# Performance work log

Measured on AMD Instinct MI355X. Metric: run time of the kernel, lower is better.

The kernel has to match this reference:

```python
import jax, jax.numpy as jnp
import numpy as np

B, H, K = 4096, 256, 16
INPUT_DIM, XPRIME_DIM = 8, 64
D = INPUT_DIM * XPRIME_DIM  # 512
LN_EPS = 1e-5


def setup_inputs() -> dict:
    key = jax.random.key(0)
    ks = jax.random.split(key, 12)
    s1 = 1.0  # Linear(1, D): fan_in=1
    sD = 1.0 / np.sqrt(D)
    sH = 1.0 / np.sqrt(H)
    return {
        "h_prev_rnn": jax.random.normal(ks[0], (B, H), jnp.float32),
        "x_l": jax.random.normal(ks[1], (B, INPUT_DIM), jnp.float32),
        "x_ext": jax.random.normal(ks[2], (B, K), jnp.float32),
        # stacked per-expert MetaNet params
        "meta_w1": jax.random.uniform(ks[3], (K, D), jnp.float32, -s1, s1),
        "meta_b1": jax.random.uniform(ks[4], (K, D), jnp.float32, -s1, s1),
        "meta_w2": jax.random.uniform(ks[5], (K, D, D), jnp.float32, -sD, sD),
        "meta_b2": jax.random.uniform(ks[6], (K, D), jnp.float32, -sD, sD),
        # gating net
        "gw1": jax.random.uniform(ks[7], (H, H), jnp.float32, -sH, sH),
        "gb1": jax.random.uniform(ks[8], (H,), jnp.float32, -sH, sH),
        "gw2": jax.random.uniform(ks[9], (H, K), jnp.float32, -sH, sH),
        "gb2": jax.random.uniform(ks[10], (K,), jnp.float32, -sH, sH),
        # LayerNorm([input_dim, xprime_dim]) affine params
        "ln_g": jnp.ones((INPUT_DIM, XPRIME_DIM), jnp.float32),
        "ln_b": jnp.zeros((INPUT_DIM, XPRIME_DIM), jnp.float32),
        "theta0": jnp.zeros((1, INPUT_DIM, XPRIME_DIM), jnp.float32),
    }


def reference(h_prev_rnn, x_l, x_ext, meta_w1, meta_b1, meta_w2, meta_b2,
              gw1, gb1, gw2, gb2, ln_g, ln_b, theta0):
    # MetaNet layer1 (Linear(1, D)): scalar input per expert -> [B, K, D]
    h1 = jnp.tanh(x_ext[:, :, None] * meta_w1[None] + meta_b1[None])
    # MetaNet layer2: per-expert DxD GEMM
    h2 = jnp.tanh(jnp.einsum('bkd,kde->bke', h1, meta_w2) + meta_b2[None])
    W = h2.reshape(h2.shape[0], K, INPUT_DIM, XPRIME_DIM)  # [B,K,i,e]
    # LayerNorm over last two dims jointly, affine
    mu = W.mean(axis=(-2, -1), keepdims=True)
    var = W.var(axis=(-2, -1), keepdims=True)
    W = (W - mu) * jax.lax.rsqrt(var + LN_EPS) * ln_g + ln_b
    # gating: softmax over experts (epoch/top_k = None path)
    logits = jnp.tanh(h_prev_rnn @ gw1 + gb1) @ gw2 + gb2
    gates = jax.nn.softmax(logits, axis=-1)  # [B, K]
    theta = jnp.einsum('bk,bkie->bie', gates, W) + theta0  # [B, i, e]
    x_prime = jnp.einsum('bi,bie->be', x_l, theta)  # [B, e]
    return (x_prime, theta)
```

## Files before the change

kernel.cpp:

```cpp
#include <hip/hip_runtime.h>
#include <stdint.h>

#define NB 4096
#define NH 256
#define NK 16
#define ND 512
#define NC 48
#define NM 48
#define RCHEB 7.0f
#define PI_F 3.14159265358979323846f
#define CCPART (NK * 2 * ND * 32)

typedef _Float16 f16;
using half8   = __attribute__((ext_vector_type(8))) _Float16;
using float4v = __attribute__((ext_vector_type(4))) float;

__device__ __forceinline__ float fast_tanh(float x) {
  float e = __builtin_amdgcn_exp2f(x * 2.88539008177793f);
  return 1.0f - 2.0f * __builtin_amdgcn_rcpf(e + 1.0f);
}

__global__ __launch_bounds__(256) void k_gs(
    const float* __restrict__ h_prev,
    const float* __restrict__ gw1, const float* __restrict__ gb1,
    const float* __restrict__ gw2, const float* __restrict__ gb2,
    const float* __restrict__ w1, const float* __restrict__ b1,
    float* __restrict__ gates, float* __restrict__ Sg, float* __restrict__ ctg) {
  __shared__ float sbuf[4096];
  const int t = threadIdx.x;
  const int blk = blockIdx.x;

  if (blk >= 512) {
    const int sb = blk - 512;
    const int k = sb >> 3;
    const int d0 = (sb & 7) * 64;
    if (sb == 0) {
      for (int i = t; i < NM * NC; i += 256) {
        const int m = i / 48, j = i - m * 48;
        const int r = (j * (2 * m + 1)) % 192;
        const float fac = (j == 0 ? 1.0f : 2.0f) * (1.0f / 48.0f);
        ctg[i] = cosf(PI_F * (float)r * (1.0f / 96.0f)) * fac;
      }
    }
    const int dl = t >> 2, mg = t & 3;
    const int d = d0 + dl;
    const float a = w1[k * ND + d];
    const float b = b1[k * ND + d];
    float o[12];
#pragma unroll
    for (int mi = 0; mi < 12; ++mi) {
      const int m = mg * 12 + mi;
      const float cx = cosf(PI_F * (float)(2 * m + 1) * (1.0f / 96.0f));
      o[mi] = fast_tanh(fmaf(a, RCHEB * cx, b));
    }
    float* dst = Sg + ((size_t)k * ND + d) * NM + mg * 12;
    *(float4*)&dst[0] = *(float4*)&o[0];
    *(float4*)&dst[4] = *(float4*)&o[4];
    *(float4*)&dst[8] = *(float4*)&o[8];
    return;
  }

  const int b0 = blk * 8;
  float* sh_h = sbuf;
  float* sh_t = sbuf + 2048;
  for (int r = 0; r < 8; ++r) sh_h[r * 256 + t] = h_prev[(b0 + r) * NH + t];
  __syncthreads();
  float acc[8];
  const float bias = gb1[t];
#pragma unroll
  for (int r = 0; r < 8; ++r) acc[r] = bias;
  for (int i = 0; i < NH; i += 4) {
    const float w0 = gw1[(i + 0) * NH + t];
    const float w1v = gw1[(i + 1) * NH + t];
    const float w2v = gw1[(i + 2) * NH + t];
    const float w3 = gw1[(i + 3) * NH + t];
#pragma unroll
    for (int r = 0; r < 8; ++r) {
      const float4 hv = *(const float4*)&sh_h[r * 256 + i];
      acc[r] += hv.x * w0 + hv.y * w1v + hv.z * w2v + hv.w * w3;
    }
  }
#pragma unroll
  for (int r = 0; r < 8; ++r) sh_t[t * 8 + r] = fast_tanh(acc[r]);
  __syncthreads();
  if (t < 128) {
    const int r = t >> 4, k = t & 15;
    float lg = gb2[k];
    for (int j = 0; j < NH; ++j) lg += sh_t[j * 8 + r] * gw2[j * NK + k];
    float m = lg;
    for (int off = 1; off < 16; off <<= 1) m = fmaxf(m, __shfl_xor(m, off, 16));
    const float e = __builtin_amdgcn_exp2f((lg - m) * 1.44269504f);
    float s = e;
    for (int off = 1; off < 16; off <<= 1) s += __shfl_xor(s, off, 16);
    gates[(b0 + r) * NK + k] = e * __builtin_amdgcn_rcpf(s);
  }
}

__global__ __launch_bounds__(256) void k_coef(
    const float* __restrict__ w2, const float* __restrict__ Sg,
    const float* __restrict__ ctg, float* __restrict__ Cc) {
  __shared__ float Gl[48][68];
  const int t = threadIdx.x;
  const int blk = blockIdx.x;
  const int k = blk >> 5;
  const int e0 = ((blk >> 2) & 7) * 64;
  const int dq = blk & 3;
  const int el = t & 63;
  const int mqu = __builtin_amdgcn_readfirstlane(t >> 6);

  const float* w2p = w2 + ((size_t)k * ND + dq * 128) * ND + e0 + el;
  const float* Sp = Sg + ((size_t)k * ND + dq * 128) * NM + mqu * 12;

  float g[12];
#pragma unroll
  for (int i = 0; i < 12; ++i) g[i] = 0.f;
#pragma unroll 4
  for (int d = 0; d < 128; ++d) {
    const float wv = w2p[(size_t)d * ND];
    const float4 s0 = *(const float4*)&Sp[d * NM];
    const float4 s1 = *(const float4*)&Sp[d * NM + 4];
    const float4 s2 = *(const float4*)&Sp[d * NM + 8];
    g[0] = fmaf(s0.x, wv, g[0]);
    g[1] = fmaf(s0.y, wv, g[1]);
    g[2] = fmaf(s0.z, wv, g[2]);
    g[3] = fmaf(s0.w, wv, g[3]);
    g[4] = fmaf(s1.x, wv, g[4]);
    g[5] = fmaf(s1.y, wv, g[5]);
    g[6] = fmaf(s1.z, wv, g[6]);
    g[7] = fmaf(s1.w, wv, g[7]);
    g[8] = fmaf(s2.x, wv, g[8]);
    g[9] = fmaf(s2.y, wv, g[9]);
    g[10] = fmaf(s2.z, wv, g[10]);
    g[11] = fmaf(s2.w, wv, g[11]);
  }

#pragma unroll
  for (int mi = 0; mi < 12; ++mi) Gl[mqu * 12 + mi][el] = g[mi];
  __syncthreads();

  float cacc[12];
#pragma unroll
  for (int i = 0; i < 12; ++i) cacc[i] = 0.f;
#pragma unroll 4
  for (int m = 0; m < NM; ++m) {
    const float gv = Gl[m][el];
    const float4 c0 = *(const float4*)&ctg[m * 48 + mqu * 12];
    const float4 c1 = *(const float4*)&ctg[m * 48 + mqu * 12 + 4];
    const float4 c2 = *(const float4*)&ctg[m * 48 + mqu * 12 + 8];
    cacc[0] = fmaf(c0.x, gv, cacc[0]);
    cacc[1] = fmaf(c0.y, gv, cacc[1]);
    cacc[2] = fmaf(c0.z, gv, cacc[2]);
    cacc[3] = fmaf(c0.w, gv, cacc[3]);
    cacc[4] = fmaf(c1.x, gv, cacc[4]);
    cacc[5] = fmaf(c1.y, gv, cacc[5]);
    cacc[6] = fmaf(c1.z, gv, cacc[6]);
    cacc[7] = fmaf(c1.w, gv, cacc[7]);
    cacc[8] = fmaf(c2.x, gv, cacc[8]);
    cacc[9] = fmaf(c2.y, gv, cacc[9]);
    cacc[10] = fmaf(c2.z, gv, cacc[10]);
    cacc[11] = fmaf(c2.w, gv, cacc[11]);
  }
  float* Ccq = Cc + (size_t)dq * CCPART;
#pragma unroll
  for (int jj = 0; jj < 12; ++jj) {
    const int j = mqu * 12 + jj;
    Ccq[((size_t)(k * 2 + (j >> 5)) * ND + e0 + el) * 32 + (j & 31)] = cacc[jj];
  }
}

__global__ __launch_bounds__(256) void k_pack(
    const float* __restrict__ Cc, const float* __restrict__ b2,
    f16* __restrict__ Cbf) {
  const int idx = blockIdx.x * 256 + threadIdx.x;
  const int flat8 = idx * 8;
  const int k2 = flat8 >> 14;
  const int rem = flat8 & 16383;
  const int e = rem >> 5, o8 = rem & 31;
  const int j0 = (k2 & 1) * 32 + o8;
  f16 o[8];
  if (j0 >= 48) {
#pragma unroll
    for (int i = 0; i < 8; ++i) o[i] = (f16)0.f;
  } else {
    float v[8];
#pragma unroll
    for (int i = 0; i < 8; ++i) v[i] = 0.f;
#pragma unroll
    for (int p = 0; p < 4; ++p) {
      const float4 u0 = *(const float4*)&Cc[(size_t)p * CCPART + flat8];
      const float4 u1 = *(const float4*)&Cc[(size_t)p * CCPART + flat8 + 4];
      v[0] += u0.x; v[1] += u0.y; v[2] += u0.z; v[3] += u0.w;
      v[4] += u1.x; v[5] += u1.y; v[6] += u1.z; v[7] += u1.w;
    }
    if (((k2 & 1) == 0) && (o8 == 0)) v[0] += b2[(k2 >> 1) * ND + e];
#pragma unroll
    for (int i = 0; i < 8; ++i) o[i] = (f16)v[i];
  }
  *(uint4*)&Cbf[flat8] = *(uint4*)o;
}

__global__ __launch_bounds__(256) void k_eval(
    const f16* __restrict__ Cbf, const float* __restrict__ gates,
    const float* __restrict__ x_ext, const float* __restrict__ x_l,
    const float* __restrict__ ln_g, const float* __restrict__ ln_b,
    const float* __restrict__ theta0, float* __restrict__ out) {
  __shared__ __align__(16) char sm[43264];
  f16* Tlds = (f16*)sm;
  float (*xp)[8][68] = (float(*)[8][68])sm;
  float (*lnbuf)[8][4][2] = (float(*)[8][4][2])(sm + 36864);
  float (*sx)[16] = (float(*)[16])(sm + 40960);
  float (*sg)[16] = (float(*)[16])(sm + 41472);
  float (*sxl)[8] = (float(*)[8])(sm + 41984);
  const int t = threadIdx.x;
  const int l = t & 63, wn = t >> 6;
  const int q = l >> 4, m16 = l & 15;
  const int b0 = blockIdx.x * 8;

  const f16* Bbase = Cbf + ((size_t)(wn * 128 + m16)) * 32 + q * 8;
  half8 BrA[16], BrB[16];
  auto loadB = [&](int k, half8(&dst)[16]) {
#pragma unroll
    for (int bni = 0; bni < 8; ++bni) {
      dst[bni * 2 + 0] =
          *(const half8*)(Bbase + ((size_t)(k * 2 + 0) * ND + bni * 16) * 32);
      dst[bni * 2 + 1] =
          *(const half8*)(Bbase + ((size_t)(k * 2 + 1) * ND + bni * 16) * 32);
    }
  };
  loadB(0, BrA);

  if (t < 128) {
    const int row = t >> 4, kk = t & 15;
    sx[row][kk] = x_ext[(b0 + row) * NK + kk];
    sg[row][kk] = gates[(b0 + row) * NK + kk];
  } else if (t < 192) {
    const int tt = t - 128;
    sxl[tt >> 3][tt & 7] = x_l[(b0 + (tt >> 3)) * 8 + (tt & 7)];
  }
  __syncthreads();

  if (t < 128) {
    const int kk = t >> 3, row = t & 7;
    f16* T0 = &Tlds[(2 * kk) * 576 + row * 36];
    f16* T1 = &Tlds[(2 * kk + 1) * 576 + row * 36];
    float u = sx[row][kk] * (1.0f / RCHEB);
    u = fminf(1.0f, fmaxf(-1.0f, u));
    const float u2 = u + u;
    float tp = 1.0f, tc = u;
    T0[0] = (f16)1.0f;
    T0[1] = (f16)u;
#pragma unroll
    for (int j = 2; j < 48; ++j) {
      const float tn = fmaf(u2, tc, -tp);
      tp = tc; tc = tn;
      if (j < 32) T0[j] = (f16)tn; else T1[j - 32] = (f16)tn;
    }
#pragma unroll
    for (int j = 48; j < 64; ++j) T1[j - 32] = (f16)0.f;
  } else {
    const int tt = t - 128;
    const int ksub = tt >> 2;
    f16* Z = &Tlds[ksub * 576 + (8 + (tt & 3) * 2) * 36];
#pragma unroll
    for (int j = 0; j < 72; ++j) Z[j] = (f16)0.f;
  }
  __syncthreads();

  float lng[8], lnb[8];
#pragma unroll
  for (int bni = 0; bni < 8; ++bni) {
    const int col = wn * 128 + bni * 16 + m16;
    lng[bni] = ln_g[col];
    lnb[bni] = ln_b[col];
  }

  float th[8][4];
#pragma unroll
  for (int bni = 0; bni < 8; ++bni)
#pragma unroll
    for (int rr = 0; rr < 4; ++rr) th[bni][rr] = 0.f;

  const f16* Abase = Tlds + m16 * 36 + q * 8;
  const float4v z = {0.f, 0.f, 0.f, 0.f};

  auto stepA = [&](int k, const half8(&Br)[16], float4v(&acc)[8],
                   float(&s)[4], float(&s2)[4]) {
    const half8 a0 = *(const half8*)(Abase + (2 * k) * 576);
    const half8 a1 = *(const half8*)(Abase + (2 * k + 1) * 576);
#pragma unroll
    for (int bni = 0; bni < 8; ++bni) {
      acc[bni] = __builtin_amdgcn_mfma_f32_16x16x32_f16(a0, Br[2 * bni], z, 0, 0, 0);
      acc[bni] = __builtin_amdgcn_mfma_f32_16x16x32_f16(a1, Br[2 * bni + 1],
                                                        acc[bni], 0, 0, 0);
    }
#pragma unroll
    for (int rr = 0; rr < 4; ++rr) { s[rr] = 0.f; s2[rr] = 0.f; }
#pragma unroll
    for (int bni = 0; bni < 8; ++bni)
#pragma unroll
      for (int rr = 0; rr < 4; ++rr) {
        const float v = fast_tanh(acc[bni][rr]);
        acc[bni][rr] = v;
        s[rr] += v;
        s2[rr] = fmaf(v, v, s2[rr]);
      }
#pragma unroll
    for (int off = 1; off < 16; off <<= 1)
#pragma unroll
      for (int rr = 0; rr < 4; ++rr) {
        s[rr] += __shfl_xor(s[rr], off, 64);
        s2[rr] += __shfl_xor(s2[rr], off, 64);
      }
  };
  auto lnwrite = [&](int k, const float(&s)[4], const float(&s2)[4]) {
    if (m16 == 0 && q < 2) {
#pragma unroll
      for (int rr = 0; rr < 4; ++rr) {
        lnbuf[k][q * 4 + rr][wn][0] = s[rr];
        lnbuf[k][q * 4 + rr][wn][1] = s2[rr];
      }
    }
  };
  auto apply = [&](int k, const float4v(&acc)[8]) {
    if (q < 2) {
#pragma unroll
      for (int rr = 0; rr < 4; ++rr) {
        const int row = q * 4 + rr;
        const float4 pa = *(const float4*)&lnbuf[k][row][0][0];
        const float4 pb = *(const float4*)&lnbuf[k][row][2][0];
        const float S1 = pa.x + pa.z + pb.x + pb.z;
        const float S2 = pa.y + pa.w + pb.y + pb.w;
        const float mu = S1 * (1.0f / 512.0f);
        const float var = fmaf(S2, 1.0f / 512.0f, -mu * mu);
        const float rs = __builtin_amdgcn_rsqf(var + 1e-5f);
        const float gate = sg[row][k];
        const float a = gate * rs;
#pragma unroll
        for (int bni = 0; bni < 8; ++bni)
          th[bni][rr] = fmaf(a * lng[bni], acc[bni][rr] - mu,
                             fmaf(gate, lnb[bni], th[bni][rr]));
      }
    }
  };

  float sA[4], s2A[4], sB[4], s2B[4];
  float4v accA[8], accB[8];

  stepA(0, BrA, accA, sA, s2A);
  lnwrite(0, sA, s2A);
  loadB(1, BrB);
  __syncthreads();
  for (int kp = 0; kp < 7; ++kp) {
    stepA(2 * kp + 1, BrB, accB, sB, s2B);
    apply(2 * kp, accA);
    lnwrite(2 * kp + 1, sB, s2B);
    loadB(2 * kp + 2, BrA);
    __syncthreads();
    stepA(2 * kp + 2, BrA, accA, sA, s2A);
    apply(2 * kp + 1, accB);
    lnwrite(2 * kp + 2, sA, s2A);
    loadB(2 * kp + 3, BrB);
    __syncthreads();
  }
  stepA(15, BrB, accB, sB, s2B);
  apply(14, accA);
  lnwrite(15, sB, s2B);
  __syncthreads();
  apply(15, accB);

  float* thbase = out + (size_t)NB * 64;
  if (q < 2) {
#pragma unroll
    for (int bni = 0; bni < 8; ++bni) {
      const int col = wn * 128 + bni * 16 + m16;
      const float t0v = theta0[col];
#pragma unroll
      for (int rr = 0; rr < 4; ++rr) {
        const float o = th[bni][rr] + t0v;
        th[bni][rr] = o;
        thbase[(size_t)(b0 + q * 4 + rr) * ND + col] = o;
      }
    }
#pragma unroll
    for (int rr = 0; rr < 4; ++rr) {
      const int row = q * 4 + rr;
      const float xlA = sxl[row][2 * wn], xlB = sxl[row][2 * wn + 1];
#pragma unroll
      for (int g4 = 0; g4 < 4; ++g4)
        xp[wn][row][g4 * 16 + m16] = xlA * th[g4][rr] + xlB * th[g4 + 4][rr];
    }
  }
  __syncthreads();
  {
    const int idx = t * 2;
    const int row = idx >> 6, ec = idx & 63;
    float2 r = {0.f, 0.f};
#pragma unroll
    for (int w4 = 0; w4 < 4; ++w4) {
      const float2 p = *(const float2*)&xp[w4][row][ec];
      r.x += p.x;
      r.y += p.y;
    }
    *(float2*)&out[(size_t)(b0 + row) * 64 + ec] = r;
  }
}

extern "C" void kernel_launch(void* const* d_in, const int* in_sizes, int n_in,
                              void* d_out, int out_size, void* d_ws, size_t ws_size,
                              hipStream_t stream) {
  const float* h_prev = (const float*)d_in[0];
  const float* x_l    = (const float*)d_in[1];
  const float* x_ext  = (const float*)d_in[2];
  const float* mw1    = (const float*)d_in[3];
  const float* mb1    = (const float*)d_in[4];
  const float* mw2    = (const float*)d_in[5];
  const float* mb2    = (const float*)d_in[6];
  const float* gw1    = (const float*)d_in[7];
  const float* gb1    = (const float*)d_in[8];
  const float* gw2    = (const float*)d_in[9];
  const float* gb2    = (const float*)d_in[10];
  const float* ln_g   = (const float*)d_in[11];
  const float* ln_b   = (const float*)d_in[12];
  const float* th0    = (const float*)d_in[13];
  float* out = (float*)d_out;

  char* ws = (char*)d_ws;
  float* gates = (float*)ws;
  f16* Cbf     = (f16*)(ws + 0x40000);
  float* Cc    = (float*)(ws + 0x140000);
  float* Sg    = (float*)(ws + 0x940000);
  float* ctg   = (float*)(ws + 0xB00000);

  hipLaunchKernelGGL(k_gs, dim3(640), dim3(256), 0, stream,
                     h_prev, gw1, gb1, gw2, gb2, mw1, mb1, gates, Sg, ctg);
  hipLaunchKernelGGL(k_coef, dim3(512), dim3(256), 0, stream,
                     mw2, Sg, ctg, Cc);
  hipLaunchKernelGGL(k_pack, dim3(256), dim3(256), 0, stream,
                     Cc, mb2, Cbf);
  hipLaunchKernelGGL(k_eval, dim3(512), dim3(256), 0, stream,
                     Cbf, gates, x_ext, x_l, ln_g, ln_b, th0, out);
}
```

Baseline: 186.0 us.

## Fill full 16-row MFMA tiles with 8 waves and DPP row reductions in k_eval

```diff
diff --git a/kernel.cpp b/kernel.cpp
--- a/kernel.cpp
+++ b/kernel.cpp
@@ -18,6 +18,20 @@
 __device__ __forceinline__ float fast_tanh(float x) {
   float e = __builtin_amdgcn_exp2f(x * 2.88539008177793f);
   return 1.0f - 2.0f * __builtin_amdgcn_rcpf(e + 1.0f);
+}
+
+template <int CTRL>
+__device__ __forceinline__ float dpp_addstep(float x) {
+  int y = __builtin_amdgcn_update_dpp(0, __builtin_bit_cast(int, x),
+                                      CTRL, 0xf, 0xf, true);
+  return x + __builtin_bit_cast(float, y);
+}
+__device__ __forceinline__ float rowsum16(float x) {
+  x = dpp_addstep<0xB1>(x);
+  x = dpp_addstep<0x4E>(x);
+  x = dpp_addstep<0x141>(x);
+  x = dpp_addstep<0x140>(x);
+  return x;
 }
 
 __global__ __launch_bounds__(256) void k_gs(
@@ -199,28 +213,28 @@
   *(uint4*)&Cbf[flat8] = *(uint4*)o;
 }
 
-__global__ __launch_bounds__(256) void k_eval(
+__global__ __launch_bounds__(512) void k_eval(
     const f16* __restrict__ Cbf, const float* __restrict__ gates,
     const float* __restrict__ x_ext, const float* __restrict__ x_l,
     const float* __restrict__ ln_g, const float* __restrict__ ln_b,
     const float* __restrict__ theta0, float* __restrict__ out) {
-  __shared__ __align__(16) char sm[43264];
+  __shared__ __align__(16) char sm[55808];
   f16* Tlds = (f16*)sm;
-  float (*xp)[8][68] = (float(*)[8][68])sm;
-  float (*lnbuf)[8][4][2] = (float(*)[8][4][2])(sm + 36864);
-  float (*sx)[16] = (float(*)[16])(sm + 40960);
-  float (*sg)[16] = (float(*)[16])(sm + 41472);
-  float (*sxl)[8] = (float(*)[8])(sm + 41984);
+  float (*xp)[16][68] = (float(*)[16][68])sm;
+  float (*lnbuf)[16][8][2] = (float(*)[16][8][2])(sm + 36864);
+  float (*sx)[16] = (float(*)[16])(sm + 53248);
+  float (*sg)[16] = (float(*)[16])(sm + 54272);
+  float (*sxl)[8] = (float(*)[8])(sm + 55296);
   const int t = threadIdx.x;
   const int l = t & 63, wn = t >> 6;
   const int q = l >> 4, m16 = l & 15;
-  const int b0 = blockIdx.x * 8;
-
-  const f16* Bbase = Cbf + ((size_t)(wn * 128 + m16)) * 32 + q * 8;
-  half8 BrA[16], BrB[16];
-  auto loadB = [&](int k, half8(&dst)[16]) {
-#pragma unroll
-    for (int bni = 0; bni < 8; ++bni) {
+  const int b0 = blockIdx.x * 16;
+
+  const f16* Bbase = Cbf + ((size_t)(wn * 64 + m16)) * 32 + q * 8;
+  half8 BrA[8], BrB[8];
+  auto loadB = [&](int k, half8(&dst)[8]) {
+#pragma unroll
+    for (int bni = 0; bni < 4; ++bni) {
       dst[bni * 2 + 0] =
           *(const half8*)(Bbase + ((size_t)(k * 2 + 0) * ND + bni * 16) * 32);
       dst[bni * 2 + 1] =
@@ -229,21 +243,20 @@
   };
   loadB(0, BrA);
 
-  if (t < 128) {
-    const int row = t >> 4, kk = t & 15;
-    sx[row][kk] = x_ext[(b0 + row) * NK + kk];
-    sg[row][kk] = gates[(b0 + row) * NK + kk];
-  } else if (t < 192) {
-    const int tt = t - 128;
+  if (t < 256) {
+    sx[t >> 4][t & 15] = x_ext[(b0 + (t >> 4)) * NK + (t & 15)];
+    sg[t >> 4][t & 15] = gates[(b0 + (t >> 4)) * NK + (t & 15)];
+  } else if (t < 384) {
+    const int tt = t - 256;
     sxl[tt >> 3][tt & 7] = x_l[(b0 + (tt >> 3)) * 8 + (tt & 7)];
   }
   __syncthreads();
 
-  if (t < 128) {
-    const int kk = t >> 3, row = t & 7;
-    f16* T0 = &Tlds[(2 * kk) * 576 + row * 36];
-    f16* T1 = &Tlds[(2 * kk + 1) * 576 + row * 36];
-    float u = sx[row][kk] * (1.0f / RCHEB);
+  if (t < 256) {
+    const int k = t >> 4, row = t & 15;
+    f16* T0 = &Tlds[(2 * k) * 576 + row * 36];
+    f16* T1 = &Tlds[(2 * k + 1) * 576 + row * 36];
+    float u = sx[row][k] * (1.0f / RCHEB);
     u = fminf(1.0f, fmaxf(-1.0f, u));
     const float u2 = u + u;
     float tp = 1.0f, tc = u;
@@ -257,38 +270,32 @@
     }
 #pragma unroll
     for (int j = 48; j < 64; ++j) T1[j - 32] = (f16)0.f;
-  } else {
-    const int tt = t - 128;
-    const int ksub = tt >> 2;
-    f16* Z = &Tlds[ksub * 576 + (8 + (tt & 3) * 2) * 36];
-#pragma unroll
-    for (int j = 0; j < 72; ++j) Z[j] = (f16)0.f;
-  }
-  __syncthreads();
-
-  float lng[8], lnb[8];
-#pragma unroll
-  for (int bni = 0; bni < 8; ++bni) {
-    const int col = wn * 128 + bni * 16 + m16;
+  }
+  __syncthreads();
+
+  float lng[4], lnb[4];
+#pragma unroll
+  for (int bni = 0; bni < 4; ++bni) {
+    const int col = wn * 64 + bni * 16 + m16;
     lng[bni] = ln_g[col];
     lnb[bni] = ln_b[col];
   }
 
-  float th[8][4];
-#pragma unroll
-  for (int bni = 0; bni < 8; ++bni)
+  float th[4][4];
+#pragma unroll
+  for (int bni = 0; bni < 4; ++bni)
 #pragma unroll
     for (int rr = 0; rr < 4; ++rr) th[bni][rr] = 0.f;
 
   const f16* Abase = Tlds + m16 * 36 + q * 8;
   const float4v z = {0.f, 0.f, 0.f, 0.f};
 
-  auto stepA = [&](int k, const half8(&Br)[16], float4v(&acc)[8],
+  auto stepA = [&](int k, const half8(&Br)[8], float4v(&acc)[4],
                    float(&s)[4], float(&s2)[4]) {
     const half8 a0 = *(const half8*)(Abase + (2 * k) * 576);
     const half8 a1 = *(const half8*)(Abase + (2 * k + 1) * 576);
 #pragma unroll
-    for (int bni = 0; bni < 8; ++bni) {
+    for (int bni = 0; bni < 4; ++bni) {
       acc[bni] = __builtin_amdgcn_mfma_f32_16x16x32_f16(a0, Br[2 * bni], z, 0, 0, 0);
       acc[bni] = __builtin_amdgcn_mfma_f32_16x16x32_f16(a1, Br[2 * bni + 1],
                                                         acc[bni], 0, 0, 0);
@@ -296,7 +303,7 @@
 #pragma unroll
     for (int rr = 0; rr < 4; ++rr) { s[rr] = 0.f; s2[rr] = 0.f; }
 #pragma unroll
-    for (int bni = 0; bni < 8; ++bni)
+    for (int bni = 0; bni < 4; ++bni)
 #pragma unroll
       for (int rr = 0; rr < 4; ++rr) {
         const float v = fast_tanh(acc[bni][rr]);
@@ -305,46 +312,42 @@
         s2[rr] = fmaf(v, v, s2[rr]);
       }
 #pragma unroll
-    for (int off = 1; off < 16; off <<= 1)
-#pragma unroll
-      for (int rr = 0; rr < 4; ++rr) {
-        s[rr] += __shfl_xor(s[rr], off, 64);
-        s2[rr] += __shfl_xor(s2[rr], off, 64);
-      }
+    for (int rr = 0; rr < 4; ++rr) {
+      s[rr] = rowsum16(s[rr]);
+      s2[rr] = rowsum16(s2[rr]);
+    }
   };
   auto lnwrite = [&](int k, const float(&s)[4], const float(&s2)[4]) {
-    if (m16 == 0 && q < 2) {
-#pragma unroll
-      for (int rr = 0; rr < 4; ++rr) {
-        lnbuf[k][q * 4 + rr][wn][0] = s[rr];
-        lnbuf[k][q * 4 + rr][wn][1] = s2[rr];
-      }
+    if (m16 == 0) {
+#pragma unroll
+      for (int rr = 0; rr < 4; ++rr)
+        *(float2*)&lnbuf[k][q * 4 + rr][wn][0] = make_float2(s[rr], s2[rr]);
     }
   };
-  auto apply = [&](int k, const float4v(&acc)[8]) {
-    if (q < 2) {
-#pragma unroll
-      for (int rr = 0; rr < 4; ++rr) {
-        const int row = q * 4 + rr;
-        const float4 pa = *(const float4*)&lnbuf[k][row][0][0];
-        const float4 pb = *(const float4*)&lnbuf[k][row][2][0];
-        const float S1 = pa.x + pa.z + pb.x + pb.z;
-        const float S2 = pa.y + pa.w + pb.y + pb.w;
-        const float mu = S1 * (1.0f / 512.0f);
-        const float var = fmaf(S2, 1.0f / 512.0f, -mu * mu);
-        const float rs = __builtin_amdgcn_rsqf(var + 1e-5f);
-        const float gate = sg[row][k];
-        const float a = gate * rs;
-#pragma unroll
-        for (int bni = 0; bni < 8; ++bni)
-          th[bni][rr] = fmaf(a * lng[bni], acc[bni][rr] - mu,
-                             fmaf(gate, lnb[bni], th[bni][rr]));
-      }
+  auto apply = [&](int k, const float4v(&acc)[4]) {
+#pragma unroll
+    for (int rr = 0; rr < 4; ++rr) {
+      const int row = q * 4 + rr;
+      const float4 pa = *(const float4*)&lnbuf[k][row][0][0];
+      const float4 pb = *(const float4*)&lnbuf[k][row][2][0];
+      const float4 pc = *(const float4*)&lnbuf[k][row][4][0];
+      const float4 pd = *(const float4*)&lnbuf[k][row][6][0];
+      const float S1 = pa.x + pa.z + pb.x + pb.z + pc.x + pc.z + pd.x + pd.z;
+      const float S2 = pa.y + pa.w + pb.y + pb.w + pc.y + pc.w + pd.y + pd.w;
+      const float mu = S1 * (1.0f / 512.0f);
+      const float var = fmaf(S2, 1.0f / 512.0f, -mu * mu);
+      const float rs = __builtin_amdgcn_rsqf(var + 1e-5f);
+      const float gate = sg[row][k];
+      const float a = gate * rs;
+#pragma unroll
+      for (int bni = 0; bni < 4; ++bni)
+        th[bni][rr] = fmaf(a * lng[bni], acc[bni][rr] - mu,
+                           fmaf(gate, lnb[bni], th[bni][rr]));
     }
   };
 
   float sA[4], s2A[4], sB[4], s2B[4];
-  float4v accA[8], accB[8];
+  float4v accA[4], accB[4];
 
   stepA(0, BrA, accA, sA, s2A);
   lnwrite(0, sA, s2A);
@@ -369,26 +372,24 @@
   apply(15, accB);
 
   float* thbase = out + (size_t)NB * 64;
-  if (q < 2) {
-#pragma unroll
-    for (int bni = 0; bni < 8; ++bni) {
-      const int col = wn * 128 + bni * 16 + m16;
-      const float t0v = theta0[col];
-#pragma unroll
-      for (int rr = 0; rr < 4; ++rr) {
-        const float o = th[bni][rr] + t0v;
-        th[bni][rr] = o;
-        thbase[(size_t)(b0 + q * 4 + rr) * ND + col] = o;
-      }
-    }
+#pragma unroll
+  for (int bni = 0; bni < 4; ++bni) {
+    const int col = wn * 64 + bni * 16 + m16;
+    const float t0v = theta0[col];
 #pragma unroll
     for (int rr = 0; rr < 4; ++rr) {
-      const int row = q * 4 + rr;
-      const float xlA = sxl[row][2 * wn], xlB = sxl[row][2 * wn + 1];
-#pragma unroll
-      for (int g4 = 0; g4 < 4; ++g4)
-        xp[wn][row][g4 * 16 + m16] = xlA * th[g4][rr] + xlB * th[g4 + 4][rr];
-    }
+      const float o = th[bni][rr] + t0v;
+      th[bni][rr] = o;
+      thbase[(size_t)(b0 + q * 4 + rr) * ND + col] = o;
+    }
+  }
+#pragma unroll
+  for (int rr = 0; rr < 4; ++rr) {
+    const int row = q * 4 + rr;
+    const float xlw = sxl[row][wn];
+#pragma unroll
+    for (int bni = 0; bni < 4; ++bni)
+      xp[wn][row][bni * 16 + m16] = xlw * th[bni][rr];
   }
   __syncthreads();
   {
@@ -396,8 +397,8 @@
     const int row = idx >> 6, ec = idx & 63;
     float2 r = {0.f, 0.f};
 #pragma unroll
-    for (int w4 = 0; w4 < 4; ++w4) {
-      const float2 p = *(const float2*)&xp[w4][row][ec];
+    for (int w8 = 0; w8 < 8; ++w8) {
+      const float2 p = *(const float2*)&xp[w8][row][ec];
       r.x += p.x;
       r.y += p.y;
     }
@@ -437,6 +438,6 @@
                      mw2, Sg, ctg, Cc);
   hipLaunchKernelGGL(k_pack, dim3(256), dim3(256), 0, stream,
                      Cc, mb2, Cbf);
-  hipLaunchKernelGGL(k_eval, dim3(512), dim3(256), 0, stream,
+  hipLaunchKernelGGL(k_eval, dim3(256), dim3(512), 0, stream,
                      Cbf, gates, x_ext, x_l, ln_g, ln_b, th0, out);
 }
```

Measured after the change: 166.9 us. 1.11x faster.
